# Kernel optimization log

Hardware: AMD Instinct MI355X
Metric: run time of the kernel (lower is better)

## Reference

```python
import jax, jax.numpy as jnp
import numpy as np

N, E, G = 50000, 800000, 500
F_IN, F_OUT, H, C = 80, 40, 20, 5


def setup_inputs() -> dict:
    key = jax.random.key(0)
    ks = jax.random.split(key, 12)
    x = jax.random.normal(ks[0], (N, F_IN), dtype=jnp.float32)
    edge_index = jax.random.randint(ks[1], (2, E), 0, N, dtype=jnp.int64)
    edge_weight = jax.random.uniform(ks[2], (E,), dtype=jnp.float32)
    batch = jnp.sort(jax.random.randint(ks[3], (N,), 0, G, dtype=jnp.int64))
    # ChebConv K=2: one Linear per Chebyshev order, shared bias
    W0 = jax.random.normal(ks[4], (F_IN, F_OUT), dtype=jnp.float32) / np.sqrt(F_IN).astype(np.float32)
    W1 = jax.random.normal(ks[5], (F_IN, F_OUT), dtype=jnp.float32) / np.sqrt(F_IN).astype(np.float32)
    b_conv = jnp.zeros((F_OUT,), dtype=jnp.float32)
    # RNN(40, 20), tanh
    W_ih = jax.random.normal(ks[6], (H, F_OUT), dtype=jnp.float32) / np.sqrt(F_OUT).astype(np.float32)
    W_hh = jax.random.normal(ks[7], (H, H), dtype=jnp.float32) / np.sqrt(H).astype(np.float32)
    b_ih = jax.random.normal(ks[8], (H,), dtype=jnp.float32) * 0.01
    b_hh = jax.random.normal(ks[9], (H,), dtype=jnp.float32) * 0.01
    # Linear(20, 5)
    W_fc = jax.random.normal(ks[10], (C, H), dtype=jnp.float32) / np.sqrt(H).astype(np.float32)
    b_fc = jax.random.normal(ks[11], (C,), dtype=jnp.float32) * 0.01
    return {"x": x, "edge_index": edge_index, "edge_weight": edge_weight,
            "batch": batch, "num_graphs": G,
            "W0": W0, "W1": W1, "b_conv": b_conv,
            "W_ih": W_ih, "W_hh": W_hh, "b_ih": b_ih, "b_hh": b_hh,
            "W_fc": W_fc, "b_fc": b_fc}


def reference(x, edge_index, edge_weight, batch, num_graphs,
              W0, W1, b_conv, W_ih, W_hh, b_ih, b_hh, W_fc, b_fc):
    n = x.shape[0]
    src, dst = edge_index[0], edge_index[1]
    # PyG ChebConv norm (sym Laplacian, lambda_max=2):
    # L_hat = 2L/lmax - I = -D^{-1/2} A D^{-1/2}; diagonal cancels to 0.
    deg = jax.ops.segment_sum(edge_weight, src, num_segments=n)
    dinv = jnp.where(deg > 0, jax.lax.rsqrt(jnp.where(deg > 0, deg, 1.0)), 0.0)
    norm = -dinv[src] * edge_weight * dinv[dst]
    # Tx0 = x ; Tx1 = L_hat x  (K=2 recursion stops here)
    Tx1 = jax.ops.segment_sum(norm[:, None] * x[src], dst, num_segments=n)  # [N,F_in]
    h = jax.nn.relu(x @ W0 + Tx1 @ W1 + b_conv)  # [N,F_out]
    # global_add_pool over graphs
    pooled = jax.ops.segment_sum(h, batch, num_segments=num_graphs)  # [G,F_out]
    # nn.RNN on 2D input => unbatched sequence of length G, h0 = 0
    def step(hprev, xt):
        hn = jnp.tanh(xt @ W_ih.T + b_ih + hprev @ W_hh.T + b_hh)
        return hn, hn
    _, seq = jax.lax.scan(step, jnp.zeros((W_hh.shape[0],), pooled.dtype), pooled)  # [G,H]
    logits = seq @ W_fc.T + b_fc  # [G,C]
    return jax.nn.log_softmax(logits, axis=1)
```

## Files before the change

### kernel.cpp

```cpp
#include <hip/hip_runtime.h>
#include <math.h>

#define NN   50000
#define NE   800000
#define NG   500
#define FIN  80
#define FOUT 40
#define HH   20
#define NC   5

#define OFF_DEG    0
#define OFF_CNT    50000
#define OFF_POOLED 100000
#define OFF_SEQ    120000
#define OFF_ROWPTR 130000
#define OFF_RANK   180004
#define OFF_ESRC   980004
#define OFF_ENORM  1780004
#define OFF_Y      2580004
#define OFF_PRE    3580004

#define TWO_LOG2E 2.8853900817779268f

__device__ __forceinline__ float tanh_pre(float y) {
    float e;
    asm("v_exp_f32 %0, %1" : "=v"(e) : "v"(y));
    float r;
    asm("v_rcp_f32 %0, %1" : "=v"(r) : "v"(e + 1.0f));
    return fmaf(-2.0f, r, 1.0f);
}

__device__ __forceinline__ float bcast_lane(float v, int k) {
    return __uint_as_float(__builtin_amdgcn_readlane(__float_as_uint(v), k));
}

__device__ __forceinline__ unsigned short bf16_rn(float f) {
    unsigned u = __float_as_uint(f);
    return (unsigned short)((u + 0x7fffu + ((u >> 16) & 1u)) >> 16);
}
__device__ __forceinline__ float bf16_to_f32(unsigned short h) {
    return __uint_as_float((unsigned)h << 16);
}

__global__ void k_degcnt(const int* __restrict__ ei, const float* __restrict__ w,
                         float* __restrict__ deg, unsigned int* __restrict__ cnt,
                         unsigned int* __restrict__ rank) {
    int e = blockIdx.x * 256 + threadIdx.x;
    if (e < NE) {
        atomicAdd(&deg[ei[e]], w[e]);
        rank[e] = atomicAdd(&cnt[ei[NE + e]], 1u);
    }
}

__global__ void k_scanptr(const unsigned int* __restrict__ cnt,
                          unsigned int* __restrict__ rowptr,
                          float* __restrict__ deg) {
    int tid = threadIdx.x;
    if (blockIdx.x > 0) {
        int n = (blockIdx.x - 1) * 1024 + tid;
        if (n < NN) {
            float d = deg[n];
            deg[n] = (d > 0.f) ? rsqrtf(d) : 0.f;
        }
        return;
    }
    __shared__ unsigned int tot[1024];
    bool act = tid < 1000;
    int beg = tid * 50;
    unsigned int vals[50];
    if (act) {
        const uint2* c2 = reinterpret_cast<const uint2*>(cnt + beg);
        #pragma unroll
        for (int j = 0; j < 25; ++j) {
            uint2 v = c2[j];
            vals[j * 2 + 0] = v.x;
            vals[j * 2 + 1] = v.y;
        }
    }
    unsigned int s = 0;
    if (act) {
        #pragma unroll
        for (int j = 0; j < 50; ++j) s += vals[j];
    }
    tot[tid] = s;
    __syncthreads();
    for (int off = 1; off < 1024; off <<= 1) {
        unsigned int t = (tid >= off) ? tot[tid - off] : 0u;
        __syncthreads();
        tot[tid] += t;
        __syncthreads();
    }
    unsigned int base = (tid > 0) ? tot[tid - 1] : 0u;
    if (act) {
        #pragma unroll
        for (int j = 0; j < 50; ++j) {
            unsigned int v = vals[j];
            vals[j] = base;
            base += v;
        }
        uint2* r2 = reinterpret_cast<uint2*>(rowptr + beg);
        #pragma unroll
        for (int j = 0; j < 25; ++j)
            r2[j] = make_uint2(vals[j * 2 + 0], vals[j * 2 + 1]);
    }
    if (tid == 1023) rowptr[NN] = tot[1023];
}

__global__ void k_y(const float* __restrict__ x, const float* __restrict__ W1,
                    const float* __restrict__ dinv, unsigned short* __restrict__ y) {
    int gid = blockIdx.x * 256 + threadIdx.x;
    if (gid >= NN * 10) return;
    int n = gid / 10;
    int c = gid % 10;
    const float* xr = x + (size_t)n * FIN;
    float a0 = 0.f, a1 = 0.f, a2 = 0.f, a3 = 0.f;
    #pragma unroll 8
    for (int f = 0; f < FIN; ++f) {
        float xf = xr[f];
        const float4 wv = *reinterpret_cast<const float4*>(W1 + f * FOUT + c * 4);
        a0 = fmaf(xf, wv.x, a0); a1 = fmaf(xf, wv.y, a1);
        a2 = fmaf(xf, wv.z, a2); a3 = fmaf(xf, wv.w, a3);
    }
    float di = dinv[n];
    ushort4 o;
    o.x = bf16_rn(a0 * di); o.y = bf16_rn(a1 * di);
    o.z = bf16_rn(a2 * di); o.w = bf16_rn(a3 * di);
    *reinterpret_cast<ushort4*>(y + (size_t)gid * 4) = o;
}

__global__ void k_fill(const int* __restrict__ ei, const float* __restrict__ w,
                       const unsigned int* __restrict__ rowptr,
                       const unsigned int* __restrict__ rank,
                       unsigned int* __restrict__ esrc, float* __restrict__ enorm) {
    int e = blockIdx.x * 256 + threadIdx.x;
    if (e >= NE) return;
    int s = ei[e];
    int d = ei[NE + e];
    unsigned int pos = rowptr[d] + rank[e];
    esrc[pos] = (unsigned int)s;
    enorm[pos] = w[e];
}

__global__ void k_gather_h(const unsigned int* __restrict__ rowptr,
                           const unsigned int* __restrict__ esrc,
                           const float* __restrict__ enorm,
                           const unsigned short* __restrict__ y,
                           const float* __restrict__ x,
                           const float* __restrict__ W0,
                           const float* __restrict__ bconv,
                           const float* __restrict__ dinv,
                           const int* __restrict__ batch,
                           float* __restrict__ pooled) {
    __shared__ float lpool[32 * FOUT];
    int tid = threadIdx.x;
    int b0 = blockIdx.x * 256;
    #pragma unroll
    for (int i = tid; i < 32 * FOUT; i += 256) lpool[i] = 0.f;
    int g_lo = batch[b0 / 10];
    __syncthreads();

    int gid = b0 + tid;
    if (gid < NN * 10) {
        int n = gid / 10;
        int c = gid % 10;
        unsigned int beg = rowptr[n], end = rowptr[n + 1];
        float z0 = 0.f, z1 = 0.f, z2 = 0.f, z3 = 0.f;
        const ushort4* y4 = reinterpret_cast<const ushort4*>(y);
        for (unsigned int k = beg; k < end; ++k) {
            unsigned int s = esrc[k];
            float nm = enorm[k];
            ushort4 yv = y4[s * 10 + c];
            z0 = fmaf(nm, bf16_to_f32(yv.x), z0);
            z1 = fmaf(nm, bf16_to_f32(yv.y), z1);
            z2 = fmaf(nm, bf16_to_f32(yv.z), z2);
            z3 = fmaf(nm, bf16_to_f32(yv.w), z3);
        }
        float mdi = -dinv[n];
        const float4 bv = *reinterpret_cast<const float4*>(bconv + c * 4);
        float a0 = bv.x, a1 = bv.y, a2 = bv.z, a3 = bv.w;
        const float* xr = x + (size_t)n * FIN;
        #pragma unroll 8
        for (int f = 0; f < FIN; ++f) {
            float xf = xr[f];
            const float4 wv = *reinterpret_cast<const float4*>(W0 + f * FOUT + c * 4);
            a0 = fmaf(xf, wv.x, a0); a1 = fmaf(xf, wv.y, a1);
            a2 = fmaf(xf, wv.z, a2); a3 = fmaf(xf, wv.w, a3);
        }
        float h0 = fmaxf(fmaf(mdi, z0, a0), 0.f);
        float h1 = fmaxf(fmaf(mdi, z1, a1), 0.f);
        float h2 = fmaxf(fmaf(mdi, z2, a2), 0.f);
        float h3 = fmaxf(fmaf(mdi, z3, a3), 0.f);
        float* lp = lpool + (batch[n] - g_lo) * FOUT + c * 4;
        atomicAdd(lp + 0, h0);
        atomicAdd(lp + 1, h1);
        atomicAdd(lp + 2, h2);
        atomicAdd(lp + 3, h3);
    }
    __syncthreads();
    int n_hi = (b0 + 255) / 10;
    if (n_hi > NN - 1) n_hi = NN - 1;
    int span = batch[n_hi] - g_lo + 1;
    for (int i = tid; i < span * FOUT; i += 256) {
        float v = lpool[i];
        if (v != 0.f) atomicAdd(&pooled[(size_t)g_lo * FOUT + i], v);
    }
}

__global__ void k_pre(const float* __restrict__ pooled, const float* __restrict__ Wih,
                      const float* __restrict__ bih, const float* __restrict__ bhh,
                      float* __restrict__ pre) {
    int gid = blockIdx.x * 256 + threadIdx.x;
    if (gid >= NG * HH) return;
    int t = gid / HH;
    int j = gid % HH;
    float acc = bih[j] + bhh[j];
    const float* pr = pooled + t * FOUT;
    const float* wr = Wih + j * FOUT;
    #pragma unroll
    for (int f = 0; f < FOUT; ++f) acc = fmaf(pr[f], wr[f], acc);
    pre[gid] = acc * TWO_LOG2E;
}

__global__ void k_tail(const float* __restrict__ pre, const float* __restrict__ Whh,
                       const float* __restrict__ Wfc, const float* __restrict__ bfc,
                       float* __restrict__ seq, float* __restrict__ out) {
    __shared__ float spre[NG * HH];
    int tid = threadIdx.x;

    {
        const float4* p4 = reinterpret_cast<const float4*>(pre);
        float4* s4 = reinterpret_cast<float4*>(spre);
        for (int i = tid; i < NG * HH / 4; i += 1024) s4[i] = p4[i];
    }
    __syncthreads();

    if (tid < 64) {
        int lane = tid;
        float whh[HH];
        #pragma unroll
        for (int k = 0; k < HH; ++k)
            whh[k] = (lane < HH) ? Whh[lane * HH + k] * TWO_LOG2E : 0.f;
        int myoff = (lane < HH) ? lane : 0;
        float h = 0.f;
        float pre_cur = spre[myoff];
        for (int t = 0; t < NG; ++t) {
            int nt = (t + 1 < NG) ? t + 1 : t;
            float pre_next = spre[nt * HH + myoff];
            float hv[HH];
            #pragma unroll
            for (int k = 0; k < HH; ++k) hv[k] = bcast_lane(h, k);
            float a0 = pre_cur, a1 = 0.f, a2 = 0.f, a3 = 0.f;
            #pragma unroll
            for (int k = 0; k < HH; k += 4) {
                a0 = fmaf(hv[k + 0], whh[k + 0], a0);
                a1 = fmaf(hv[k + 1], whh[k + 1], a1);
                a2 = fmaf(hv[k + 2], whh[k + 2], a2);
                a3 = fmaf(hv[k + 3], whh[k + 3], a3);
            }
            h = tanh_pre((a0 + a1) + (a2 + a3));
            if (lane < HH) seq[t * HH + lane] = h;
            pre_cur = pre_next;
        }
    }
    __syncthreads();

    if (tid < NG) {
        float s[HH];
        #pragma unroll
        for (int j = 0; j < HH; ++j) s[j] = seq[tid * HH + j];
        float lg[NC];
        float m = -1e30f;
        #pragma unroll
        for (int c = 0; c < NC; ++c) {
            float acc = bfc[c];
            #pragma unroll
            for (int j = 0; j < HH; ++j) acc = fmaf(s[j], Wfc[c * HH + j], acc);
            lg[c] = acc;
            m = fmaxf(m, acc);
        }
        float lse = 0.f;
        #pragma unroll
        for (int c = 0; c < NC; ++c) lse += expf(lg[c] - m);
        lse = logf(lse);
        #pragma unroll
        for (int c = 0; c < NC; ++c) out[tid * NC + c] = lg[c] - m - lse;
    }
}

extern "C" void kernel_launch(void* const* d_in, const int* in_sizes, int n_in,
                              void* d_out, int out_size, void* d_ws, size_t ws_size,
                              hipStream_t stream) {
    const float* x     = (const float*)d_in[0];
    const int*   ei    = (const int*)  d_in[1];
    const float* w     = (const float*)d_in[2];
    const int*   batch = (const int*)  d_in[3];
    const float* W0    = (const float*)d_in[5];
    const float* W1    = (const float*)d_in[6];
    const float* bconv = (const float*)d_in[7];
    const float* Wih   = (const float*)d_in[8];
    const float* Whh   = (const float*)d_in[9];
    const float* bih   = (const float*)d_in[10];
    const float* bhh   = (const float*)d_in[11];
    const float* Wfc   = (const float*)d_in[12];
    const float* bfc   = (const float*)d_in[13];
    float* out = (float*)d_out;

    float*          ws     = (float*)d_ws;
    float*          deg    = ws + OFF_DEG;
    unsigned int*   cnt    = (unsigned int*)(ws + OFF_CNT);
    float*          pooled = ws + OFF_POOLED;
    float*          seq    = ws + OFF_SEQ;
    unsigned int*   rowptr = (unsigned int*)(ws + OFF_ROWPTR);
    unsigned int*   rank   = (unsigned int*)(ws + OFF_RANK);
    unsigned int*   esrc   = (unsigned int*)(ws + OFF_ESRC);
    float*          enorm  = ws + OFF_ENORM;
    unsigned short* y      = (unsigned short*)(ws + OFF_Y);
    float*          pre    = ws + OFF_PRE;

    hipMemsetAsync(d_ws, 0, (size_t)(OFF_POOLED + NG * FOUT) * sizeof(float), stream);

    k_degcnt<<<(NE + 255) / 256, 256, 0, stream>>>(ei, w, deg, cnt, rank);
    k_scanptr<<<50, 1024, 0, stream>>>(cnt, rowptr, deg);
    k_y<<<(NN * 10 + 255) / 256, 256, 0, stream>>>(x, W1, deg, y);
    k_fill<<<(NE + 255) / 256, 256, 0, stream>>>(ei, w, rowptr, rank, esrc, enorm);
    k_gather_h<<<(NN * 10 + 255) / 256, 256, 0, stream>>>(rowptr, esrc, enorm, y, x,
                                                          W0, bconv, deg, batch, pooled);
    k_pre<<<(NG * HH + 255) / 256, 256, 0, stream>>>(pooled, Wih, bih, bhh, pre);
    k_tail<<<1, 1024, 0, stream>>>(pre, Whh, Wfc, bfc, seq, out);
}
```

Measured before the change: 261.7 us.

## Fuse degree counting with x@W1 projection and pack full edge norm records

The x@W1 projection no longer depends on dinv, so it is merged into the degree/count kernel as extra blocks, which removes one launch and lets the dense work overlap with the atomics. The full symmetric norm is now computed per edge in the fill kernel and stored with the source index as a packed uint2 record. The gather then reads one 8-byte load per edge instead of two separate arrays and skips the per-node dinv scaling. In exchange, fill does two extra random dinv reads per edge, and applying dinv[src] after bf16 rounding of y shifts rounding slightly.

```diff
diff --git a/kernel.cpp b/kernel.cpp
--- a/kernel.cpp
+++ b/kernel.cpp
@@ -9,14 +9,16 @@
 #define HH   20
 #define NC   5
 
+#define NB_EDGE 3125
+#define NB_Y    1954
+
 #define OFF_DEG    0
 #define OFF_CNT    50000
 #define OFF_POOLED 100000
 #define OFF_SEQ    120000
 #define OFF_ROWPTR 130000
 #define OFF_RANK   180004
-#define OFF_ESRC   980004
-#define OFF_ENORM  1780004
+#define OFF_REC    980004
 #define OFF_Y      2580004
 #define OFF_PRE    3580004
 
@@ -42,73 +44,22 @@
     return __uint_as_float((unsigned)h << 16);
 }
 
-__global__ void k_degcnt(const int* __restrict__ ei, const float* __restrict__ w,
-                         float* __restrict__ deg, unsigned int* __restrict__ cnt,
-                         unsigned int* __restrict__ rank) {
-    int e = blockIdx.x * 256 + threadIdx.x;
-    if (e < NE) {
-        atomicAdd(&deg[ei[e]], w[e]);
-        rank[e] = atomicAdd(&cnt[ei[NE + e]], 1u);
-    }
-}
-
-__global__ void k_scanptr(const unsigned int* __restrict__ cnt,
-                          unsigned int* __restrict__ rowptr,
-                          float* __restrict__ deg) {
+__global__ void k_degcnt_y(const int* __restrict__ ei, const float* __restrict__ w,
+                           float* __restrict__ deg, unsigned int* __restrict__ cnt,
+                           unsigned int* __restrict__ rank,
+                           const float* __restrict__ x, const float* __restrict__ W1,
+                           unsigned short* __restrict__ y) {
+    int b = blockIdx.x;
     int tid = threadIdx.x;
-    if (blockIdx.x > 0) {
-        int n = (blockIdx.x - 1) * 1024 + tid;
-        if (n < NN) {
-            float d = deg[n];
-            deg[n] = (d > 0.f) ? rsqrtf(d) : 0.f;
+    if (b < NB_EDGE) {
+        int e = b * 256 + tid;
+        if (e < NE) {
+            atomicAdd(&deg[ei[e]], w[e]);
+            rank[e] = atomicAdd(&cnt[ei[NE + e]], 1u);
         }
         return;
     }
-    __shared__ unsigned int tot[1024];
-    bool act = tid < 1000;
-    int beg = tid * 50;
-    unsigned int vals[50];
-    if (act) {
-        const uint2* c2 = reinterpret_cast<const uint2*>(cnt + beg);
-        #pragma unroll
-        for (int j = 0; j < 25; ++j) {
-            uint2 v = c2[j];
-            vals[j * 2 + 0] = v.x;
-            vals[j * 2 + 1] = v.y;
-        }
-    }
-    unsigned int s = 0;
-    if (act) {
-        #pragma unroll
-        for (int j = 0; j < 50; ++j) s += vals[j];
-    }
-    tot[tid] = s;
-    __syncthreads();
-    for (int off = 1; off < 1024; off <<= 1) {
-        unsigned int t = (tid >= off) ? tot[tid - off] : 0u;
-        __syncthreads();
-        tot[tid] += t;
-        __syncthreads();
-    }
-    unsigned int base = (tid > 0) ? tot[tid - 1] : 0u;
-    if (act) {
-        #pragma unroll
-        for (int j = 0; j < 50; ++j) {
-            unsigned int v = vals[j];
-            vals[j] = base;
-            base += v;
-        }
-        uint2* r2 = reinterpret_cast<uint2*>(rowptr + beg);
-        #pragma unroll
-        for (int j = 0; j < 25; ++j)
-            r2[j] = make_uint2(vals[j * 2 + 0], vals[j * 2 + 1]);
-    }
-    if (tid == 1023) rowptr[NN] = tot[1023];
-}
-
-__global__ void k_y(const float* __restrict__ x, const float* __restrict__ W1,
-                    const float* __restrict__ dinv, unsigned short* __restrict__ y) {
-    int gid = blockIdx.x * 256 + threadIdx.x;
+    int gid = (b - NB_EDGE) * 256 + tid;
     if (gid >= NN * 10) return;
     int n = gid / 10;
     int c = gid % 10;
@@ -121,34 +72,85 @@
         a0 = fmaf(xf, wv.x, a0); a1 = fmaf(xf, wv.y, a1);
         a2 = fmaf(xf, wv.z, a2); a3 = fmaf(xf, wv.w, a3);
     }
-    float di = dinv[n];
     ushort4 o;
-    o.x = bf16_rn(a0 * di); o.y = bf16_rn(a1 * di);
-    o.z = bf16_rn(a2 * di); o.w = bf16_rn(a3 * di);
+    o.x = bf16_rn(a0); o.y = bf16_rn(a1); o.z = bf16_rn(a2); o.w = bf16_rn(a3);
     *reinterpret_cast<ushort4*>(y + (size_t)gid * 4) = o;
 }
 
+__global__ void k_scanptr(const unsigned int* __restrict__ cnt,
+                          unsigned int* __restrict__ rowptr,
+                          float* __restrict__ deg) {
+    int tid = threadIdx.x;
+    if (blockIdx.x > 0) {
+        int n = (blockIdx.x - 1) * 1024 + tid;
+        if (n < NN) {
+            float d = deg[n];
+            deg[n] = (d > 0.f) ? rsqrtf(d) : 0.f;
+        }
+        return;
+    }
+    __shared__ unsigned int tot[1024];
+    bool act = tid < 1000;
+    int beg = tid * 50;
+    unsigned int vals[50];
+    if (act) {
+        const uint2* c2 = reinterpret_cast<const uint2*>(cnt + beg);
+        #pragma unroll
+        for (int j = 0; j < 25; ++j) {
+            uint2 v = c2[j];
+            vals[j * 2 + 0] = v.x;
+            vals[j * 2 + 1] = v.y;
+        }
+    }
+    unsigned int s = 0;
+    if (act) {
+        #pragma unroll
+        for (int j = 0; j < 50; ++j) s += vals[j];
+    }
+    tot[tid] = s;
+    __syncthreads();
+    for (int off = 1; off < 1024; off <<= 1) {
+        unsigned int t = (tid >= off) ? tot[tid - off] : 0u;
+        __syncthreads();
+        tot[tid] += t;
+        __syncthreads();
+    }
+    unsigned int base = (tid > 0) ? tot[tid - 1] : 0u;
+    if (act) {
+        #pragma unroll
+        for (int j = 0; j < 50; ++j) {
+            unsigned int v = vals[j];
+            vals[j] = base;
+            base += v;
+        }
+        uint2* r2 = reinterpret_cast<uint2*>(rowptr + beg);
+        #pragma unroll
+        for (int j = 0; j < 25; ++j)
+            r2[j] = make_uint2(vals[j * 2 + 0], vals[j * 2 + 1]);
+    }
+    if (tid == 1023) rowptr[NN] = tot[1023];
+}
+
 __global__ void k_fill(const int* __restrict__ ei, const float* __restrict__ w,
+                       const float* __restrict__ dinv,
                        const unsigned int* __restrict__ rowptr,
                        const unsigned int* __restrict__ rank,
-                       unsigned int* __restrict__ esrc, float* __restrict__ enorm) {
+                       uint2* __restrict__ rec) {
     int e = blockIdx.x * 256 + threadIdx.x;
     if (e >= NE) return;
     int s = ei[e];
     int d = ei[NE + e];
+    float nm = -dinv[s] * w[e] * dinv[d];
     unsigned int pos = rowptr[d] + rank[e];
-    esrc[pos] = (unsigned int)s;
-    enorm[pos] = w[e];
+    rec[pos] = make_uint2((unsigned int)s, __float_as_uint(nm));
 }
 
 __global__ void k_gather_h(const unsigned int* __restrict__ rowptr,
-                           const unsigned int* __restrict__ esrc,
-                           const float* __restrict__ enorm,
+                           const uint2* __restrict__ rec,
                            const unsigned short* __restrict__ y,
                            const float* __restrict__ x,
                            const float* __restrict__ W0,
                            const float* __restrict__ bconv,
-                           const float* __restrict__ dinv,
                            const int* __restrict__ batch,
                            float* __restrict__ pooled) {
     __shared__ float lpool[32 * FOUT];
@@ -167,17 +169,16 @@
         float z0 = 0.f, z1 = 0.f, z2 = 0.f, z3 = 0.f;
         const ushort4* y4 = reinterpret_cast<const ushort4*>(y);
         for (unsigned int k = beg; k < end; ++k) {
-            unsigned int s = esrc[k];
-            float nm = enorm[k];
-            ushort4 yv = y4[s * 10 + c];
+            uint2 r = rec[k];
+            float nm = __uint_as_float(r.y);
+            ushort4 yv = y4[r.x * 10 + c];
             z0 = fmaf(nm, bf16_to_f32(yv.x), z0);
             z1 = fmaf(nm, bf16_to_f32(yv.y), z1);
             z2 = fmaf(nm, bf16_to_f32(yv.z), z2);
             z3 = fmaf(nm, bf16_to_f32(yv.w), z3);
         }
-        float mdi = -dinv[n];
         const float4 bv = *reinterpret_cast<const float4*>(bconv + c * 4);
-        float a0 = bv.x, a1 = bv.y, a2 = bv.z, a3 = bv.w;
+        float a0 = bv.x + z0, a1 = bv.y + z1, a2 = bv.z + z2, a3 = bv.w + z3;
         const float* xr = x + (size_t)n * FIN;
         #pragma unroll 8
         for (int f = 0; f < FIN; ++f) {
@@ -186,10 +187,10 @@
             a0 = fmaf(xf, wv.x, a0); a1 = fmaf(xf, wv.y, a1);
             a2 = fmaf(xf, wv.z, a2); a3 = fmaf(xf, wv.w, a3);
         }
-        float h0 = fmaxf(fmaf(mdi, z0, a0), 0.f);
-        float h1 = fmaxf(fmaf(mdi, z1, a1), 0.f);
-        float h2 = fmaxf(fmaf(mdi, z2, a2), 0.f);
-        float h3 = fmaxf(fmaf(mdi, z3, a3), 0.f);
+        float h0 = fmaxf(a0, 0.f);
+        float h1 = fmaxf(a1, 0.f);
+        float h2 = fmaxf(a2, 0.f);
+        float h3 = fmaxf(a3, 0.f);
         float* lp = lpool + (batch[n] - g_lo) * FOUT + c * 4;
         atomicAdd(lp + 0, h0);
         atomicAdd(lp + 1, h1);
@@ -312,19 +313,17 @@
     float*          seq    = ws + OFF_SEQ;
     unsigned int*   rowptr = (unsigned int*)(ws + OFF_ROWPTR);
     unsigned int*   rank   = (unsigned int*)(ws + OFF_RANK);
-    unsigned int*   esrc   = (unsigned int*)(ws + OFF_ESRC);
-    float*          enorm  = ws + OFF_ENORM;
+    uint2*          rec    = (uint2*)(ws + OFF_REC);
     unsigned short* y      = (unsigned short*)(ws + OFF_Y);
     float*          pre    = ws + OFF_PRE;
 
     hipMemsetAsync(d_ws, 0, (size_t)(OFF_POOLED + NG * FOUT) * sizeof(float), stream);
 
-    k_degcnt<<<(NE + 255) / 256, 256, 0, stream>>>(ei, w, deg, cnt, rank);
+    k_degcnt_y<<<NB_EDGE + NB_Y, 256, 0, stream>>>(ei, w, deg, cnt, rank, x, W1, y);
     k_scanptr<<<50, 1024, 0, stream>>>(cnt, rowptr, deg);
-    k_y<<<(NN * 10 + 255) / 256, 256, 0, stream>>>(x, W1, deg, y);
-    k_fill<<<(NE + 255) / 256, 256, 0, stream>>>(ei, w, rowptr, rank, esrc, enorm);
-    k_gather_h<<<(NN * 10 + 255) / 256, 256, 0, stream>>>(rowptr, esrc, enorm, y, x,
-                                                          W0, bconv, deg, batch, pooled);
+    k_fill<<<(NE + 255) / 256, 256, 0, stream>>>(ei, w, deg, rowptr, rank, rec);
+    k_gather_h<<<(NN * 10 + 255) / 256, 256, 0, stream>>>(rowptr, rec, y, x,
+                                                          W0, bconv, batch, pooled);
     k_pre<<<(NG * HH + 255) / 256, 256, 0, stream>>>(pooled, Wih, bih, bhh, pre);
     k_tail<<<1, 1024, 0, stream>>>(pre, Whh, Wfc, bfc, seq, out);
 }
```

After: 250.9 us. 1.04x faster.
